# Optimization experiments

Measured on AMD Instinct MI355X. Metric: run time of the kernel, lower is better.

The kernel has to match this reference:

```python
import jax, jax.numpy as jnp
import numpy as np
import math

DIM = 1024
NUM_HEADS = 16
HEAD_DIM = DIM // NUM_HEADS
B, S = 2, 2048

def setup_inputs() -> dict:
    key = jax.random.key(0)
    ks = jax.random.split(key, 9)
    sc = 0.02
    return {
        "x": jax.random.normal(ks[0], (B, S, DIM), jnp.float32),
        "Wq": jax.random.normal(ks[1], (DIM, DIM), jnp.float32) * sc,
        "bq": jax.random.normal(ks[2], (DIM,), jnp.float32) * sc,
        "Wk": jax.random.normal(ks[3], (DIM, DIM), jnp.float32) * sc,
        "bk": jax.random.normal(ks[4], (DIM,), jnp.float32) * sc,
        "Wv": jax.random.normal(ks[5], (DIM, DIM), jnp.float32) * sc,
        "bv": jax.random.normal(ks[6], (DIM,), jnp.float32) * sc,
        "Wo": jax.random.normal(ks[7], (DIM, DIM), jnp.float32) * sc,
        "bo": jax.random.normal(ks[8], (DIM,), jnp.float32) * sc,
    }

def reference(x, Wq, bq, Wk, bk, Wv, bv, Wo, bo):
    b, s, d = x.shape
    h, hd = NUM_HEADS, HEAD_DIM
    # qkv projections: [B,S,D] -> [B,H,S,hd]
    def split_heads(t):
        return t.reshape(b, s, h, hd).transpose(0, 2, 1, 3)
    q = split_heads(x @ Wq + bq)
    k = split_heads(x @ Wk + bk)
    v = split_heads(x @ Wv + bv)
    # scores [B,H,S,S], scale, causal mask via where(-10000), softmax
    scores = jnp.einsum('bhqd,bhkd->bhqk', q, k) / math.sqrt(hd)
    causal = jnp.tril(jnp.ones((s, s), dtype=bool))  # [S,S]
    scores = jnp.where(causal[None, None], scores, jnp.asarray(-10000.0, scores.dtype))
    probs = jax.nn.softmax(scores, axis=-1)
    ctx = jnp.einsum('bhqk,bhkd->bhqd', probs, v)
    ctx = ctx.transpose(0, 2, 1, 3).reshape(b, s, d)
    return ctx @ Wo + bo
```

## Files before the change

kernel.cpp:

```cpp
#include <hip/hip_runtime.h>
#include <hip/hip_bf16.h>

#define DIM 1024
#define NUM_HEADS 16
#define HEAD_DIM 64
#define BATCH 2
#define SEQ 2048
#define M_ROWS (BATCH * SEQ)

typedef short bh8 __attribute__((ext_vector_type(8)));
typedef float f32x4 __attribute__((ext_vector_type(4)));
typedef float f32x16 __attribute__((ext_vector_type(16)));

#define SCALE_Q 0.18033688011116016f

#define MFMA16(a, b, c) __builtin_amdgcn_mfma_f32_16x16x32_bf16(a, b, c, 0, 0, 0)
#define MFMA32(a, b, c) __builtin_amdgcn_mfma_f32_32x32x16_bf16(a, b, c, 0, 0, 0)

#if __has_builtin(__builtin_amdgcn_exp2f)
#define EXP2F(x) __builtin_amdgcn_exp2f(x)
#else
#define EXP2F(x) exp2f(x)
#endif

__device__ __forceinline__ ushort f2bf(float f) {
    union { float f; unsigned u; } v; v.f = f;
    unsigned u = v.u;
    unsigned r = (u + 0x7FFFu + ((u >> 16) & 1u)) >> 16;
    return (ushort)r;
}

__device__ __forceinline__ unsigned cvt_pk_bf16(float lo, float hi) {
    unsigned r;
    asm("v_cvt_pk_bf16_f32 %0, %1, %2" : "=v"(r) : "v"(lo), "v"(hi));
    return r;
}

__device__ __forceinline__ void plane_swap(unsigned a, unsigned b,
                                           unsigned& o0, unsigned& o1, int h) {
#if __has_builtin(__builtin_amdgcn_permlane32_swap)
    (void)h;
    auto pr = __builtin_amdgcn_permlane32_swap(a, b, false, false);
    unsigned o[2]; __builtin_memcpy(o, &pr, 8);
    o0 = o[0]; o1 = o[1];
#else
    unsigned sa = (unsigned)__shfl_xor((int)a, 32);
    unsigned sb = (unsigned)__shfl_xor((int)b, 32);
    o0 = h ? sb : a;
    o1 = h ? b : sa;
#endif
}

__device__ __forceinline__ void async_cp16(const ushort* g, ushort* l) {
    __builtin_amdgcn_global_load_lds(
        (const __attribute__((address_space(1))) void*)(uintptr_t)g,
        (__attribute__((address_space(3))) void*)(uint32_t)(uintptr_t)l,
        16, 0, 0);
}

__global__ __launch_bounds__(256) void prep_inputs(
    const float* __restrict__ W0, const float* __restrict__ W1,
    const float* __restrict__ W2, const float* __restrict__ W3,
    const float* __restrict__ x,
    ushort* __restrict__ T0, ushort* __restrict__ T1,
    ushort* __restrict__ T2, ushort* __restrict__ T3,
    ushort* __restrict__ xb)
{
    const int z = blockIdx.z;
    const int t = threadIdx.x;
    if (z == 4) {
        int base = (blockIdx.y * 32 + blockIdx.x) * 1024 + t;
        const float4* in4 = (const float4*)x;
        ushort4* out4 = (ushort4*)xb;
        #pragma unroll
        for (int i = 0; i < 4; ++i) {
            float4 v = in4[base + i * 256];
            ushort4 o;
            o.x = f2bf(v.x); o.y = f2bf(v.y); o.z = f2bf(v.z); o.w = f2bf(v.w);
            out4[base + i * 256] = o;
        }
        return;
    }
    __shared__ float tile[32][33];
    const float* W = (z == 0) ? W0 : (z == 1) ? W1 : (z == 2) ? W2 : W3;
    ushort* Wt = (z == 0) ? T0 : (z == 1) ? T1 : (z == 2) ? T2 : T3;
    const int tx = t & 31, ty = t >> 5;
    const int k0 = blockIdx.y * 32, n0 = blockIdx.x * 32;
    #pragma unroll
    for (int i = 0; i < 4; ++i)
        tile[ty + 8 * i][tx] = W[(size_t)(k0 + ty + 8 * i) * DIM + n0 + tx];
    __syncthreads();
    #pragma unroll
    for (int i = 0; i < 4; ++i)
        Wt[(size_t)(n0 + ty + 8 * i) * DIM + k0 + tx] = f2bf(tile[tx][ty + 8 * i]);
}

#define GTM 128
#define GTN 64
#define GBK 64

__device__ __forceinline__ void gemm_core(
    const ushort* __restrict__ A, const ushort* __restrict__ Bt,
    ushort* smem, int m0, int n0, int t, f32x4 acc[4][2])
{
    ushort* As = smem;
    ushort* Bs = smem + 8192;
    const int lane = t & 63, wave = t >> 6;
    const int col = lane & 15, quad = lane >> 4;
    const int wm = (wave & 1) * 64, wn = (wave >> 1) * 32;

    for (int k0 = 0; k0 < DIM; k0 += GBK) {
        __syncthreads();
        #pragma unroll
        for (int j = 0; j < 4; ++j) {
            int C = wave * 256 + j * 64 + lane;
            int row = C >> 3;
            int lch = (C & 7) ^ (row & 7);
            async_cp16(&A[(size_t)(m0 + row) * DIM + k0 + lch * 8],
                       &As[(wave * 256 + j * 64) * 8]);
        }
        #pragma unroll
        for (int j = 0; j < 2; ++j) {
            int C = wave * 128 + j * 64 + lane;
            int row = C >> 3;
            int lch = (C & 7) ^ (row & 7);
            async_cp16(&Bt[(size_t)(n0 + row) * DIM + k0 + lch * 8],
                       &Bs[(wave * 128 + j * 64) * 8]);
        }
        __syncthreads();
        #pragma unroll
        for (int kk = 0; kk < 2; ++kk) {
            bh8 af[4], bfr[2];
            #pragma unroll
            for (int mi = 0; mi < 4; ++mi) {
                int row = wm + mi * 16 + col;
                af[mi] = *(const bh8*)&As[row * 64 + (((kk * 4 + quad) ^ (row & 7)) * 8)];
            }
            #pragma unroll
            for (int ni = 0; ni < 2; ++ni) {
                int row = wn + ni * 16 + col;
                bfr[ni] = *(const bh8*)&Bs[row * 64 + (((kk * 4 + quad) ^ (row & 7)) * 8)];
            }
            #pragma unroll
            for (int mi = 0; mi < 4; ++mi)
                #pragma unroll
                for (int ni = 0; ni < 2; ++ni)
                    acc[mi][ni] = MFMA16(af[mi], bfr[ni], acc[mi][ni]);
        }
    }
}

__global__ __launch_bounds__(256) void gemm_qkv(
    const ushort* __restrict__ A,
    const ushort* __restrict__ WqT, const ushort* __restrict__ WkT,
    const ushort* __restrict__ WvT,
    const float* __restrict__ bq, const float* __restrict__ bk,
    const float* __restrict__ bv,
    ushort* __restrict__ qo, ushort* __restrict__ ko_, ushort* __restrict__ vo)
{
    __shared__ ushort smem[12288];
    const int z = blockIdx.z;
    const ushort* Bt = (z == 0) ? WqT : (z == 1) ? WkT : WvT;
    const float* bias = (z == 0) ? bq : (z == 1) ? bk : bv;
    ushort* outp = (z == 0) ? qo : (z == 1) ? ko_ : vo;

    const int t = threadIdx.x;
    const int lane = t & 63, wave = t >> 6;
    const int col = lane & 15, quad = lane >> 4;
    const int m0 = blockIdx.y * GTM, n0 = blockIdx.x * GTN;
    const int wm = (wave & 1) * 64, wn = (wave >> 1) * 32;
    f32x4 acc[4][2] = {};

    gemm_core(A, Bt, smem, m0, n0, t, acc);

    const int b = m0 >> 11, s0 = m0 & (SEQ - 1);
    const int h = n0 >> 6;

    if (z < 2) {
        const float scl = (z == 0) ? SCALE_Q : 1.f;
        __syncthreads();
        ushort* LT = smem;
        #pragma unroll
        for (int mi = 0; mi < 4; ++mi)
            #pragma unroll
            for (int ni = 0; ni < 2; ++ni) {
                int dl = wn + ni * 16 + col;
                float bvv = bias[n0 + dl];
                #pragma unroll
                for (int r = 0; r < 4; ++r) {
                    int ml = wm + mi * 16 + quad * 4 + r;
                    LT[ml * 72 + dl] = f2bf((acc[mi][ni][r] + bvv) * scl);
                }
            }
        __syncthreads();
        ushort* Cp = outp + (((size_t)(b * NUM_HEADS + h) * SEQ + s0) << 6);
        #pragma unroll
        for (int i = 0; i < 4; ++i) {
            int c = i * 256 + t;
            int row = c >> 3, ko = (c & 7) * 8;
            *(uint4*)&Cp[row * 64 + ko] = *(const uint4*)&LT[row * 72 + ko];
        }
    } else {
        __syncthreads();
        ushort* LT = smem;
        #pragma unroll
        for (int mi = 0; mi < 4; ++mi)
            #pragma unroll
            for (int ni = 0; ni < 2; ++ni) {
                int nl = wn + ni * 16 + col;
                float bvv = bias[n0 + nl];
                #pragma unroll
                for (int r = 0; r < 4; ++r) {
                    int ml = wm + mi * 16 + quad * 4 + r;
                    LT[nl * 136 + ml] = f2bf(acc[mi][ni][r] + bvv);
                }
            }
        __syncthreads();
        ushort* Cp = outp + (((size_t)(b * NUM_HEADS + h) * HEAD_DIM) << 11);
        #pragma unroll
        for (int i = 0; i < 4; ++i) {
            int c = i * 256 + t;
            int row = c >> 4, mo = (c & 15) * 8;
            *(uint4*)&Cp[((size_t)row << 11) + s0 + mo] = *(const uint4*)&LT[row * 136 + mo];
        }
    }
}

__global__ __launch_bounds__(256) void gemm_out(
    const ushort* __restrict__ A, const ushort* __restrict__ Bt,
    const float* __restrict__ bias, float* __restrict__ C)
{
    __shared__ ushort smem[12288];
    const int t = threadIdx.x;
    const int lane = t & 63, wave = t >> 6;
    const int col = lane & 15, quad = lane >> 4;
    const int m0 = blockIdx.y * GTM, n0 = blockIdx.x * GTN;
    const int wm = (wave & 1) * 64, wn = (wave >> 1) * 32;
    f32x4 acc[4][2] = {};

    gemm_core(A, Bt, smem, m0, n0, t, acc);

    #pragma unroll
    for (int mi = 0; mi < 4; ++mi)
        #pragma unroll
        for (int ni = 0; ni < 2; ++ni) {
            int n = n0 + wn + ni * 16 + col;
            float bvv = bias[n];
            #pragma unroll
            for (int r = 0; r < 4; ++r) {
                int m = m0 + wm + mi * 16 + quad * 4 + r;
                C[(size_t)m * DIM + n] = acc[mi][ni][r] + bvv;
            }
        }
}

__global__ __launch_bounds__(256, 2) void attn_mfma(
    const ushort* __restrict__ Qg, const ushort* __restrict__ Kg,
    const ushort* __restrict__ Vtg, ushort* __restrict__ ctx)
{
    __shared__ char smem[34304];
    float* OA   = (float*)smem;
    float* OB   = (float*)(smem + 16640);
    float* lbuf = (float*)(smem + 33280);

    const int t = threadIdx.x;
    const int lane = t & 63, wave = t >> 6;
    const int q32 = lane & 31, h = lane >> 5;
    const int bh = blockIdx.x & 31;
    const int pi = blockIdx.x >> 5;
    const int b = bh >> 4, hd = bh & 15;
    const int kw0 = wave * 32;
    const ushort* Kp = Kg + ((size_t)bh << 17);
    const ushort* Vp = Vtg + ((size_t)bh << 17);
    const ushort* Qp0 = Qg + ((size_t)bh << 17);

    #pragma unroll 1
    for (int ph = 0; ph < 2; ++ph) {
        const int qt = ph ? pi : (31 - pi);
        const int q0 = qt << 6;

        bh8 qf[2][4];
        #pragma unroll
        for (int qti = 0; qti < 2; ++qti)
            #pragma unroll
            for (int kc = 0; kc < 4; ++kc)
                qf[qti][kc] = *(const bh8*)&Qp0[((size_t)(q0 + qti * 32 + q32) << 6)
                                                + kc * 16 + h * 8];

        f32x16 O[2][2] = {};
        float l[2] = {0.f, 0.f};
        const int nIter = (q0 + 191) >> 7;

        bh8 kf_n[4], vf_n[2][2];
        #pragma unroll
        for (int kc = 0; kc < 4; ++kc)
            kf_n[kc] = *(const bh8*)&Kp[((size_t)(kw0 + q32) << 6) + kc * 16 + h * 8];
        #pragma unroll
        for (int dti = 0; dti < 2; ++dti)
            #pragma unroll
            for (int kc = 0; kc < 2; ++kc)
                vf_n[dti][kc] = *(const bh8*)&Vp[((size_t)(dti * 32 + q32) << 11)
                                                 + kw0 + kc * 16 + h * 8];

        #pragma unroll 1
        for (int it = 0; it < nIter; ++it) {
            const int kb = it << 7;
            bh8 kf[4], vf[2][2];
            #pragma unroll
            for (int kc = 0; kc < 4; ++kc) kf[kc] = kf_n[kc];
            #pragma unroll
            for (int dti = 0; dti < 2; ++dti) {
                vf[dti][0] = vf_n[dti][0]; vf[dti][1] = vf_n[dti][1];
            }

            if (it + 1 < nIter) {
                const int kb2 = kb + 128;
                #pragma unroll
                for (int kc = 0; kc < 4; ++kc)
                    kf_n[kc] = *(const bh8*)&Kp[((size_t)(kb2 + kw0 + q32) << 6)
                                                + kc * 16 + h * 8];
                #pragma unroll
                for (int dti = 0; dti < 2; ++dti)
                    #pragma unroll
                    for (int kc = 0; kc < 2; ++kc)
                        vf_n[dti][kc] = *(const bh8*)&Vp[((size_t)(dti * 32 + q32) << 11)
                                                         + kb2 + kw0 + kc * 16 + h * 8];
            }

            if (kb + kw0 > q0 + 63) continue;

            f32x16 St[2] = {};
            #pragma unroll
            for (int kc = 0; kc < 4; ++kc) {
                St[0] = MFMA32(kf[kc], qf[0][kc], St[0]);
                St[1] = MFMA32(kf[kc], qf[1][kc], St[1]);
            }

            if (kb + kw0 + 31 > q0) {
                #pragma unroll
                for (int qti = 0; qti < 2; ++qti) {
                    int q_abs = q0 + qti * 32 + q32;
                    #pragma unroll
                    for (int r = 0; r < 16; ++r) {
                        int key_abs = kb + kw0 + (r & 3) + ((r >> 2) << 3) + 4 * h;
                        if (key_abs > q_abs) St[qti][r] = -1e30f;
                    }
                }
            }

            #pragma unroll
            for (int qti = 0; qti < 2; ++qti) {
                float p[16];
                #pragma unroll
                for (int r = 0; r < 16; ++r) p[r] = EXP2F(St[qti][r]);
                float t0 = (p[0] + p[1]) + (p[2] + p[3]);
                float t1 = (p[4] + p[5]) + (p[6] + p[7]);
                float t2 = (p[8] + p[9]) + (p[10] + p[11]);
                float t3 = (p[12] + p[13]) + (p[14] + p[15]);
                l[qti] += (t0 + t1) + (t2 + t3);

                unsigned w[8];
                #pragma unroll
                for (int m = 0; m < 8; ++m) w[m] = cvt_pk_bf16(p[2 * m], p[2 * m + 1]);
                unsigned j0, j1, j2, j3, j4, j5, j6, j7;
                plane_swap(w[0], w[2], j0, j2, h);
                plane_swap(w[1], w[3], j1, j3, h);
                plane_swap(w[4], w[6], j4, j6, h);
                plane_swap(w[5], w[7], j5, j7, h);
                union { unsigned u[4]; bh8 v; } pu0, pu1;
                pu0.u[0] = j0; pu0.u[1] = j1; pu0.u[2] = j2; pu0.u[3] = j3;
                pu1.u[0] = j4; pu1.u[1] = j5; pu1.u[2] = j6; pu1.u[3] = j7;

                O[qti][0] = MFMA32(vf[0][0], pu0.v, O[qti][0]);
                O[qti][1] = MFMA32(vf[1][0], pu0.v, O[qti][1]);
                O[qti][0] = MFMA32(vf[0][1], pu1.v, O[qti][0]);
                O[qti][1] = MFMA32(vf[1][1], pu1.v, O[qti][1]);
            }
        }

        l[0] += __shfl_xor(l[0], 32);
        l[1] += __shfl_xor(l[1], 32);
        if (lane < 32) {
            lbuf[wave * 64 + q32]      = l[0];
            lbuf[wave * 64 + 32 + q32] = l[1];
        }
        __syncthreads();

        if (wave == 1 || wave == 3) {
            float* dst = (wave == 1) ? OA : OB;
            #pragma unroll
            for (int qti = 0; qti < 2; ++qti)
                #pragma unroll
                for (int dti = 0; dti < 2; ++dti)
                    #pragma unroll
                    for (int r = 0; r < 16; ++r) {
                        int d_l = dti * 32 + (r & 3) + ((r >> 2) << 3) + 4 * h;
                        dst[d_l * 65 + qti * 32 + q32] = O[qti][dti][r];
                    }
        }
        __syncthreads();
        if (wave == 0 || wave == 2) {
            float* src = (wave == 0) ? OA : OB;
            #pragma unroll
            for (int qti = 0; qti < 2; ++qti)
                #pragma unroll
                for (int dti = 0; dti < 2; ++dti)
                    #pragma unroll
                    for (int r = 0; r < 16; ++r) {
                        int d_l = dti * 32 + (r & 3) + ((r >> 2) << 3) + 4 * h;
                        O[qti][dti][r] += src[d_l * 65 + qti * 32 + q32];
                    }
        }
        __syncthreads();
        if (wave == 2) {
            #pragma unroll
            for (int qti = 0; qti < 2; ++qti)
                #pragma unroll
                for (int dti = 0; dti < 2; ++dti)
                    #pragma unroll
                    for (int r = 0; r < 16; ++r) {
                        int d_l = dti * 32 + (r & 3) + ((r >> 2) << 3) + 4 * h;
                        OA[d_l * 65 + qti * 32 + q32] = O[qti][dti][r];
                    }
        }
        __syncthreads();
        if (wave == 0) {
            float tot0 = lbuf[q32] + lbuf[64 + q32] + lbuf[128 + q32] + lbuf[192 + q32];
            float tot1 = lbuf[32 + q32] + lbuf[96 + q32] + lbuf[160 + q32] + lbuf[224 + q32];
            float inv0 = 1.f / tot0, inv1 = 1.f / tot1;
            ushort* Oq = (ushort*)(smem + 16640);
            #pragma unroll
            for (int qti = 0; qti < 2; ++qti) {
                float invq = qti ? inv1 : inv0;
                int qrow = qti * 32 + q32;
                #pragma unroll
                for (int dti = 0; dti < 2; ++dti)
                    #pragma unroll
                    for (int rg = 0; rg < 4; ++rg) {
                        int d0 = dti * 32 + rg * 8 + 4 * h;
                        float s0 = (O[qti][dti][rg * 4 + 0] + OA[(d0 + 0) * 65 + qrow]) * invq;
                        float s1 = (O[qti][dti][rg * 4 + 1] + OA[(d0 + 1) * 65 + qrow]) * invq;
                        float s2 = (O[qti][dti][rg * 4 + 2] + OA[(d0 + 2) * 65 + qrow]) * invq;
                        float s3 = (O[qti][dti][rg * 4 + 3] + OA[(d0 + 3) * 65 + qrow]) * invq;
                        uint2 pk; pk.x = cvt_pk_bf16(s0, s1); pk.y = cvt_pk_bf16(s2, s3);
                        *(uint2*)&Oq[qrow * 72 + d0] = pk;
                    }
            }
            #pragma unroll
            for (int i = 0; i < 8; ++i) {
                int c = i * 64 + lane;
                int row = c >> 3, ko = (c & 7) * 8;
                *(uint4*)&ctx[((size_t)(b * SEQ) + q0 + row) * DIM + (hd << 6) + ko] =
                    *(const uint4*)&Oq[row * 72 + ko];
            }
        }
        __syncthreads();
    }
}

extern "C" void kernel_launch(void* const* d_in, const int* in_sizes, int n_in,
                              void* d_out, int out_size, void* d_ws, size_t ws_size,
                              hipStream_t stream) {
    const float* x  = (const float*)d_in[0];
    const float* Wq = (const float*)d_in[1];
    const float* bq = (const float*)d_in[2];
    const float* Wk = (const float*)d_in[3];
    const float* bk = (const float*)d_in[4];
    const float* Wv = (const float*)d_in[5];
    const float* bv = (const float*)d_in[6];
    const float* Wo = (const float*)d_in[7];
    const float* bo = (const float*)d_in[8];
    float* out = (float*)d_out;

    ushort* x_bf   = (ushort*)d_ws;
    ushort* wq_t   = x_bf + 4194304;
    ushort* wk_t   = wq_t + 1048576;
    ushort* wv_t   = wk_t + 1048576;
    ushort* wo_t   = wv_t + 1048576;
    ushort* q_ws   = wo_t + 1048576;
    ushort* k_ws   = q_ws + 4194304;
    ushort* vt_ws  = k_ws + 4194304;
    ushort* ctx_ws = vt_ws + 4194304;

    dim3 pgrid(32, 32, 5);
    prep_inputs<<<pgrid, 256, 0, stream>>>(Wq, Wk, Wv, Wo, x,
                                           wq_t, wk_t, wv_t, wo_t, x_bf);

    dim3 qkv_grid(DIM / GTN, M_ROWS / GTM, 3);
    gemm_qkv<<<qkv_grid, 256, 0, stream>>>(x_bf, wq_t, wk_t, wv_t,
                                           bq, bk, bv, q_ws, k_ws, vt_ws);

    attn_mfma<<<512, 256, 0, stream>>>(q_ws, k_ws, vt_ws, ctx_ws);

    dim3 ogrid(DIM / GTN, M_ROWS / GTM);
    gemm_out<<<ogrid, 256, 0, stream>>>(ctx_ws, wo_t, bo, out);
}
```

Measured before the change: 192.1 us.

## Shrink attention query tile to 32 rows, launch 4x more blocks, drop phase pairing

The attention kernel now gives each block a single 32-row query tile instead of two paired 64-row tiles, and the grid grows from 512 to 2048 blocks. Shared memory is halved and launch bounds raised to 4 blocks per SM to lift occupancy. Heaviest tiles are scheduled first to balance the causal triangle, and the loop now breaks early instead of continuing. K/V are reloaded into the same registers rather than double-buffered, but each block reuses K/V across only half as many queries, so per-row K/V traffic goes up.

```diff
diff --git a/kernel.cpp b/kernel.cpp
--- a/kernel.cpp
+++ b/kernel.cpp
@@ -254,207 +254,169 @@
         }
 }
 
-__global__ __launch_bounds__(256, 2) void attn_mfma(
+__global__ __launch_bounds__(256, 4) void attn_mfma(
     const ushort* __restrict__ Qg, const ushort* __restrict__ Kg,
     const ushort* __restrict__ Vtg, ushort* __restrict__ ctx)
 {
-    __shared__ char smem[34304];
+    __shared__ char smem[17408];
     float* OA   = (float*)smem;
-    float* OB   = (float*)(smem + 16640);
-    float* lbuf = (float*)(smem + 33280);
+    float* OB   = (float*)(smem + 8448);
+    float* lbuf = (float*)(smem + 16896);
 
     const int t = threadIdx.x;
     const int lane = t & 63, wave = t >> 6;
     const int q32 = lane & 31, h = lane >> 5;
     const int bh = blockIdx.x & 31;
-    const int pi = blockIdx.x >> 5;
+    const int qt = 63 - (blockIdx.x >> 5);
     const int b = bh >> 4, hd = bh & 15;
+    const int q0 = qt << 5;
     const int kw0 = wave * 32;
     const ushort* Kp = Kg + ((size_t)bh << 17);
     const ushort* Vp = Vtg + ((size_t)bh << 17);
-    const ushort* Qp0 = Qg + ((size_t)bh << 17);
+    const ushort* Qp = Qg + ((size_t)bh << 17);
+
+    bh8 qf[4];
+    #pragma unroll
+    for (int kc = 0; kc < 4; ++kc)
+        qf[kc] = *(const bh8*)&Qp[((size_t)(q0 + q32) << 6) + kc * 16 + h * 8];
+
+    f32x16 O[2] = {};
+    float l = 0.f;
+    const int nIter = (q0 + 159) >> 7;
+
+    bh8 kf[4], vf[2][2];
+    #pragma unroll
+    for (int kc = 0; kc < 4; ++kc)
+        kf[kc] = *(const bh8*)&Kp[((size_t)(kw0 + q32) << 6) + kc * 16 + h * 8];
+    #pragma unroll
+    for (int dti = 0; dti < 2; ++dti)
+        #pragma unroll
+        for (int kc = 0; kc < 2; ++kc)
+            vf[dti][kc] = *(const bh8*)&Vp[((size_t)(dti * 32 + q32) << 11)
+                                           + kw0 + kc * 16 + h * 8];
 
     #pragma unroll 1
-    for (int ph = 0; ph < 2; ++ph) {
-        const int qt = ph ? pi : (31 - pi);
-        const int q0 = qt << 6;
-
-        bh8 qf[2][4];
-        #pragma unroll
-        for (int qti = 0; qti < 2; ++qti)
+    for (int it = 0; it < nIter; ++it) {
+        const int kb = it << 7;
+        if (kb + kw0 > q0 + 31) break;
+
+        f32x16 St = {};
+        #pragma unroll
+        for (int kc = 0; kc < 4; ++kc)
+            St = MFMA32(kf[kc], qf[kc], St);
+
+        const int kb2 = kb + 128;
+        if (it + 1 < nIter) {
             #pragma unroll
             for (int kc = 0; kc < 4; ++kc)
-                qf[qti][kc] = *(const bh8*)&Qp0[((size_t)(q0 + qti * 32 + q32) << 6)
-                                                + kc * 16 + h * 8];
-
-        f32x16 O[2][2] = {};
-        float l[2] = {0.f, 0.f};
-        const int nIter = (q0 + 191) >> 7;
-
-        bh8 kf_n[4], vf_n[2][2];
-        #pragma unroll
-        for (int kc = 0; kc < 4; ++kc)
-            kf_n[kc] = *(const bh8*)&Kp[((size_t)(kw0 + q32) << 6) + kc * 16 + h * 8];
+                kf[kc] = *(const bh8*)&Kp[((size_t)(kb2 + kw0 + q32) << 6)
+                                          + kc * 16 + h * 8];
+        }
+
+        if (kb + kw0 + 31 > q0) {
+            int q_abs = q0 + q32;
+            #pragma unroll
+            for (int r = 0; r < 16; ++r) {
+                int key_abs = kb + kw0 + (r & 3) + ((r >> 2) << 3) + 4 * h;
+                if (key_abs > q_abs) St[r] = -1e30f;
+            }
+        }
+
+        float p[16];
+        #pragma unroll
+        for (int r = 0; r < 16; ++r) p[r] = EXP2F(St[r]);
+        float t0 = (p[0] + p[1]) + (p[2] + p[3]);
+        float t1 = (p[4] + p[5]) + (p[6] + p[7]);
+        float t2 = (p[8] + p[9]) + (p[10] + p[11]);
+        float t3 = (p[12] + p[13]) + (p[14] + p[15]);
+        l += (t0 + t1) + (t2 + t3);
+
+        unsigned w[8];
+        #pragma unroll
+        for (int m = 0; m < 8; ++m) w[m] = cvt_pk_bf16(p[2 * m], p[2 * m + 1]);
+        unsigned j0, j1, j2, j3, j4, j5, j6, j7;
+        plane_swap(w[0], w[2], j0, j2, h);
+        plane_swap(w[1], w[3], j1, j3, h);
+        plane_swap(w[4], w[6], j4, j6, h);
+        plane_swap(w[5], w[7], j5, j7, h);
+        union { unsigned u[4]; bh8 v; } pu0, pu1;
+        pu0.u[0] = j0; pu0.u[1] = j1; pu0.u[2] = j2; pu0.u[3] = j3;
+        pu1.u[0] = j4; pu1.u[1] = j5; pu1.u[2] = j6; pu1.u[3] = j7;
+
+        O[0] = MFMA32(vf[0][0], pu0.v, O[0]);
+        O[1] = MFMA32(vf[1][0], pu0.v, O[1]);
+        O[0] = MFMA32(vf[0][1], pu1.v, O[0]);
+        O[1] = MFMA32(vf[1][1], pu1.v, O[1]);
+
+        if (it + 1 < nIter) {
+            #pragma unroll
+            for (int dti = 0; dti < 2; ++dti)
+                #pragma unroll
+                for (int kc = 0; kc < 2; ++kc)
+                    vf[dti][kc] = *(const bh8*)&Vp[((size_t)(dti * 32 + q32) << 11)
+                                                   + kb2 + kw0 + kc * 16 + h * 8];
+        }
+    }
+
+    l += __shfl_xor(l, 32);
+    if (h == 0) lbuf[wave * 32 + q32] = l;
+    __syncthreads();
+
+    if (wave == 1 || wave == 3) {
+        float* dst = (wave == 1) ? OA : OB;
         #pragma unroll
         for (int dti = 0; dti < 2; ++dti)
             #pragma unroll
-            for (int kc = 0; kc < 2; ++kc)
-                vf_n[dti][kc] = *(const bh8*)&Vp[((size_t)(dti * 32 + q32) << 11)
-                                                 + kw0 + kc * 16 + h * 8];
-
-        #pragma unroll 1
-        for (int it = 0; it < nIter; ++it) {
-            const int kb = it << 7;
-            bh8 kf[4], vf[2][2];
-            #pragma unroll
-            for (int kc = 0; kc < 4; ++kc) kf[kc] = kf_n[kc];
-            #pragma unroll
-            for (int dti = 0; dti < 2; ++dti) {
-                vf[dti][0] = vf_n[dti][0]; vf[dti][1] = vf_n[dti][1];
-            }
-
-            if (it + 1 < nIter) {
-                const int kb2 = kb + 128;
-                #pragma unroll
-                for (int kc = 0; kc < 4; ++kc)
-                    kf_n[kc] = *(const bh8*)&Kp[((size_t)(kb2 + kw0 + q32) << 6)
-                                                + kc * 16 + h * 8];
-                #pragma unroll
-                for (int dti = 0; dti < 2; ++dti)
-                    #pragma unroll
-                    for (int kc = 0; kc < 2; ++kc)
-                        vf_n[dti][kc] = *(const bh8*)&Vp[((size_t)(dti * 32 + q32) << 11)
-                                                         + kb2 + kw0 + kc * 16 + h * 8];
-            }
-
-            if (kb + kw0 > q0 + 63) continue;
-
-            f32x16 St[2] = {};
-            #pragma unroll
-            for (int kc = 0; kc < 4; ++kc) {
-                St[0] = MFMA32(kf[kc], qf[0][kc], St[0]);
-                St[1] = MFMA32(kf[kc], qf[1][kc], St[1]);
-            }
-
-            if (kb + kw0 + 31 > q0) {
-                #pragma unroll
-                for (int qti = 0; qti < 2; ++qti) {
-                    int q_abs = q0 + qti * 32 + q32;
-                    #pragma unroll
-                    for (int r = 0; r < 16; ++r) {
-                        int key_abs = kb + kw0 + (r & 3) + ((r >> 2) << 3) + 4 * h;
-                        if (key_abs > q_abs) St[qti][r] = -1e30f;
-                    }
-                }
-            }
-
-            #pragma unroll
-            for (int qti = 0; qti < 2; ++qti) {
-                float p[16];
-                #pragma unroll
-                for (int r = 0; r < 16; ++r) p[r] = EXP2F(St[qti][r]);
-                float t0 = (p[0] + p[1]) + (p[2] + p[3]);
-                float t1 = (p[4] + p[5]) + (p[6] + p[7]);
-                float t2 = (p[8] + p[9]) + (p[10] + p[11]);
-                float t3 = (p[12] + p[13]) + (p[14] + p[15]);
-                l[qti] += (t0 + t1) + (t2 + t3);
-
-                unsigned w[8];
-                #pragma unroll
-                for (int m = 0; m < 8; ++m) w[m] = cvt_pk_bf16(p[2 * m], p[2 * m + 1]);
-                unsigned j0, j1, j2, j3, j4, j5, j6, j7;
-                plane_swap(w[0], w[2], j0, j2, h);
-                plane_swap(w[1], w[3], j1, j3, h);
-                plane_swap(w[4], w[6], j4, j6, h);
-                plane_swap(w[5], w[7], j5, j7, h);
-                union { unsigned u[4]; bh8 v; } pu0, pu1;
-                pu0.u[0] = j0; pu0.u[1] = j1; pu0.u[2] = j2; pu0.u[3] = j3;
-                pu1.u[0] = j4; pu1.u[1] = j5; pu1.u[2] = j6; pu1.u[3] = j7;
-
-                O[qti][0] = MFMA32(vf[0][0], pu0.v, O[qti][0]);
-                O[qti][1] = MFMA32(vf[1][0], pu0.v, O[qti][1]);
-                O[qti][0] = MFMA32(vf[0][1], pu1.v, O[qti][0]);
-                O[qti][1] = MFMA32(vf[1][1], pu1.v, O[qti][1]);
-            }
-        }
-
-        l[0] += __shfl_xor(l[0], 32);
-        l[1] += __shfl_xor(l[1], 32);
-        if (lane < 32) {
-            lbuf[wave * 64 + q32]      = l[0];
-            lbuf[wave * 64 + 32 + q32] = l[1];
-        }
-        __syncthreads();
-
-        if (wave == 1 || wave == 3) {
-            float* dst = (wave == 1) ? OA : OB;
-            #pragma unroll
-            for (int qti = 0; qti < 2; ++qti)
-                #pragma unroll
-                for (int dti = 0; dti < 2; ++dti)
-                    #pragma unroll
-                    for (int r = 0; r < 16; ++r) {
-                        int d_l = dti * 32 + (r & 3) + ((r >> 2) << 3) + 4 * h;
-                        dst[d_l * 65 + qti * 32 + q32] = O[qti][dti][r];
-                    }
-        }
-        __syncthreads();
-        if (wave == 0 || wave == 2) {
-            float* src = (wave == 0) ? OA : OB;
-            #pragma unroll
-            for (int qti = 0; qti < 2; ++qti)
-                #pragma unroll
-                for (int dti = 0; dti < 2; ++dti)
-                    #pragma unroll
-                    for (int r = 0; r < 16; ++r) {
-                        int d_l = dti * 32 + (r & 3) + ((r >> 2) << 3) + 4 * h;
-                        O[qti][dti][r] += src[d_l * 65 + qti * 32 + q32];
-                    }
-        }
-        __syncthreads();
-        if (wave == 2) {
-            #pragma unroll
-            for (int qti = 0; qti < 2; ++qti)
-                #pragma unroll
-                for (int dti = 0; dti < 2; ++dti)
-                    #pragma unroll
-                    for (int r = 0; r < 16; ++r) {
-                        int d_l = dti * 32 + (r & 3) + ((r >> 2) << 3) + 4 * h;
-                        OA[d_l * 65 + qti * 32 + q32] = O[qti][dti][r];
-                    }
-        }
-        __syncthreads();
-        if (wave == 0) {
-            float tot0 = lbuf[q32] + lbuf[64 + q32] + lbuf[128 + q32] + lbuf[192 + q32];
-            float tot1 = lbuf[32 + q32] + lbuf[96 + q32] + lbuf[160 + q32] + lbuf[224 + q32];
-            float inv0 = 1.f / tot0, inv1 = 1.f / tot1;
-            ushort* Oq = (ushort*)(smem + 16640);
-            #pragma unroll
-            for (int qti = 0; qti < 2; ++qti) {
-                float invq = qti ? inv1 : inv0;
-                int qrow = qti * 32 + q32;
-                #pragma unroll
-                for (int dti = 0; dti < 2; ++dti)
-                    #pragma unroll
-                    for (int rg = 0; rg < 4; ++rg) {
-                        int d0 = dti * 32 + rg * 8 + 4 * h;
-                        float s0 = (O[qti][dti][rg * 4 + 0] + OA[(d0 + 0) * 65 + qrow]) * invq;
-                        float s1 = (O[qti][dti][rg * 4 + 1] + OA[(d0 + 1) * 65 + qrow]) * invq;
-                        float s2 = (O[qti][dti][rg * 4 + 2] + OA[(d0 + 2) * 65 + qrow]) * invq;
-                        float s3 = (O[qti][dti][rg * 4 + 3] + OA[(d0 + 3) * 65 + qrow]) * invq;
-                        uint2 pk; pk.x = cvt_pk_bf16(s0, s1); pk.y = cvt_pk_bf16(s2, s3);
-                        *(uint2*)&Oq[qrow * 72 + d0] = pk;
-                    }
-            }
-            #pragma unroll
-            for (int i = 0; i < 8; ++i) {
-                int c = i * 64 + lane;
-                int row = c >> 3, ko = (c & 7) * 8;
-                *(uint4*)&ctx[((size_t)(b * SEQ) + q0 + row) * DIM + (hd << 6) + ko] =
-                    *(const uint4*)&Oq[row * 72 + ko];
-            }
-        }
-        __syncthreads();
+            for (int r = 0; r < 16; ++r) {
+                int d_l = dti * 32 + (r & 3) + ((r >> 2) << 3) + 4 * h;
+                dst[d_l * 33 + q32] = O[dti][r];
+            }
+    }
+    __syncthreads();
+    if (wave == 0 || wave == 2) {
+        float* src = (wave == 0) ? OA : OB;
+        #pragma unroll
+        for (int dti = 0; dti < 2; ++dti)
+            #pragma unroll
+            for (int r = 0; r < 16; ++r) {
+                int d_l = dti * 32 + (r & 3) + ((r >> 2) << 3) + 4 * h;
+                O[dti][r] += src[d_l * 33 + q32];
+            }
+    }
+    __syncthreads();
+    if (wave == 2) {
+        #pragma unroll
+        for (int dti = 0; dti < 2; ++dti)
+            #pragma unroll
+            for (int r = 0; r < 16; ++r) {
+                int d_l = dti * 32 + (r & 3) + ((r >> 2) << 3) + 4 * h;
+                OA[d_l * 33 + q32] = O[dti][r];
+            }
+    }
+    __syncthreads();
+    if (wave == 0) {
+        float tot = lbuf[q32] + lbuf[32 + q32] + lbuf[64 + q32] + lbuf[96 + q32];
+        float inv = 1.f / tot;
+        ushort* Oq = (ushort*)(smem + 8448);
+        #pragma unroll
+        for (int dti = 0; dti < 2; ++dti)
+            #pragma unroll
+            for (int rg = 0; rg < 4; ++rg) {
+                int d0 = dti * 32 + rg * 8 + 4 * h;
+                float s0 = (O[dti][rg * 4 + 0] + OA[(d0 + 0) * 33 + q32]) * inv;
+                float s1 = (O[dti][rg * 4 + 1] + OA[(d0 + 1) * 33 + q32]) * inv;
+                float s2 = (O[dti][rg * 4 + 2] + OA[(d0 + 2) * 33 + q32]) * inv;
+                float s3 = (O[dti][rg * 4 + 3] + OA[(d0 + 3) * 33 + q32]) * inv;
+                uint2 pk; pk.x = cvt_pk_bf16(s0, s1); pk.y = cvt_pk_bf16(s2, s3);
+                *(uint2*)&Oq[q32 * 72 + d0] = pk;
+            }
+        #pragma unroll
+        for (int i = 0; i < 4; ++i) {
+            int c = i * 64 + lane;
+            int row = c >> 3, ko = (c & 7) * 8;
+            *(uint4*)&ctx[((size_t)(b * SEQ) + q0 + row) * DIM + (hd << 6) + ko] =
+                *(const uint4*)&Oq[row * 72 + ko];
+        }
     }
 }
 
@@ -490,7 +452,7 @@
     gemm_qkv<<<qkv_grid, 256, 0, stream>>>(x_bf, wq_t, wk_t, wv_t,
                                            bq, bk, bv, q_ws, k_ws, vt_ws);
 
-    attn_mfma<<<512, 256, 0, stream>>>(q_ws, k_ws, vt_ws, ctx_ws);
+    attn_mfma<<<2048, 256, 0, stream>>>(q_ws, k_ws, vt_ws, ctx_ws);
 
     dim3 ogrid(DIM / GTN, M_ROWS / GTM);
     gemm_out<<<ogrid, 256, 0, stream>>>(ctx_ws, wo_t, bo, out);
```

New measurement: 209.2 us. 8.9% more time.

## Split paired attention q-tiles into separate blocks and swizzle GEMM block order

Applied to the files above, without the earlier changes.

The attention kernel previously had each block process two q-tiles (a long and a short one, for causal load balancing). It now launches 1024 blocks that each handle a single q-tile, ordered longest-first, and breaks out of the key loop early instead of continuing. The V prefetch is moved after the PV MFMAs to shorten register live ranges. The QKV and output GEMMs remap block indices with an XCD-style swizzle so that neighbouring tiles land on the same chiplet and share L2. The cost is lost explicit pairing, with load balance left to the hardware scheduler.

```diff
diff --git a/kernel.cpp b/kernel.cpp
--- a/kernel.cpp
+++ b/kernel.cpp
@@ -159,7 +159,10 @@
     ushort* __restrict__ qo, ushort* __restrict__ ko_, ushort* __restrict__ vo)
 {
     __shared__ ushort smem[12288];
-    const int z = blockIdx.z;
+    const int lin = blockIdx.x + 16 * blockIdx.y + 512 * blockIdx.z;
+    const int swz = (lin & 7) * 192 + (lin >> 3);
+    const int bx = swz & 15, by = (swz >> 4) & 31, z = swz >> 9;
+
     const ushort* Bt = (z == 0) ? WqT : (z == 1) ? WkT : WvT;
     const float* bias = (z == 0) ? bq : (z == 1) ? bk : bv;
     ushort* outp = (z == 0) ? qo : (z == 1) ? ko_ : vo;
@@ -167,7 +170,7 @@
     const int t = threadIdx.x;
     const int lane = t & 63, wave = t >> 6;
     const int col = lane & 15, quad = lane >> 4;
-    const int m0 = blockIdx.y * GTM, n0 = blockIdx.x * GTN;
+    const int m0 = by * GTM, n0 = bx * GTN;
     const int wm = (wave & 1) * 64, wn = (wave >> 1) * 32;
     f32x4 acc[4][2] = {};
 
@@ -231,10 +234,14 @@
     const float* __restrict__ bias, float* __restrict__ C)
 {
     __shared__ ushort smem[12288];
+    const int lin = blockIdx.x + 16 * blockIdx.y;
+    const int swz = (lin & 7) * 64 + (lin >> 3);
+    const int bx = swz & 15, by = swz >> 4;
+
     const int t = threadIdx.x;
     const int lane = t & 63, wave = t >> 6;
     const int col = lane & 15, quad = lane >> 4;
-    const int m0 = blockIdx.y * GTM, n0 = blockIdx.x * GTN;
+    const int m0 = by * GTM, n0 = bx * GTN;
     const int wm = (wave & 1) * 64, wn = (wave >> 1) * 32;
     f32x4 acc[4][2] = {};
 
@@ -267,194 +274,187 @@
     const int lane = t & 63, wave = t >> 6;
     const int q32 = lane & 31, h = lane >> 5;
     const int bh = blockIdx.x & 31;
-    const int pi = blockIdx.x >> 5;
+    const int qt = 31 - (blockIdx.x >> 5);
     const int b = bh >> 4, hd = bh & 15;
+    const int q0 = qt << 6;
     const int kw0 = wave * 32;
     const ushort* Kp = Kg + ((size_t)bh << 17);
     const ushort* Vp = Vtg + ((size_t)bh << 17);
-    const ushort* Qp0 = Qg + ((size_t)bh << 17);
+    const ushort* Qp = Qg + ((size_t)bh << 17);
+
+    bh8 qf[2][4];
+    #pragma unroll
+    for (int qti = 0; qti < 2; ++qti)
+        #pragma unroll
+        for (int kc = 0; kc < 4; ++kc)
+            qf[qti][kc] = *(const bh8*)&Qp[((size_t)(q0 + qti * 32 + q32) << 6)
+                                           + kc * 16 + h * 8];
+
+    f32x16 O[2][2] = {};
+    float l[2] = {0.f, 0.f};
+    const int nIter = (q0 + 191) >> 7;
+
+    bh8 kf_n[4], vf[2][2];
+    #pragma unroll
+    for (int kc = 0; kc < 4; ++kc)
+        kf_n[kc] = *(const bh8*)&Kp[((size_t)(kw0 + q32) << 6) + kc * 16 + h * 8];
+    #pragma unroll
+    for (int dti = 0; dti < 2; ++dti)
+        #pragma unroll
+        for (int kc = 0; kc < 2; ++kc)
+            vf[dti][kc] = *(const bh8*)&Vp[((size_t)(dti * 32 + q32) << 11)
+                                           + kw0 + kc * 16 + h * 8];
 
     #pragma unroll 1
-    for (int ph = 0; ph < 2; ++ph) {
-        const int qt = ph ? pi : (31 - pi);
-        const int q0 = qt << 6;
-
-        bh8 qf[2][4];
+    for (int it = 0; it < nIter; ++it) {
+        const int kb = it << 7;
+        if (kb + kw0 > q0 + 63) break;
+
+        bh8 kf[4];
+        #pragma unroll
+        for (int kc = 0; kc < 4; ++kc) kf[kc] = kf_n[kc];
+
+        const int kb2 = kb + 128;
+        if (it + 1 < nIter) {
+            #pragma unroll
+            for (int kc = 0; kc < 4; ++kc)
+                kf_n[kc] = *(const bh8*)&Kp[((size_t)(kb2 + kw0 + q32) << 6)
+                                            + kc * 16 + h * 8];
+        }
+
+        f32x16 St[2] = {};
+        #pragma unroll
+        for (int kc = 0; kc < 4; ++kc) {
+            St[0] = MFMA32(kf[kc], qf[0][kc], St[0]);
+            St[1] = MFMA32(kf[kc], qf[1][kc], St[1]);
+        }
+
+        if (kb + kw0 + 31 > q0) {
+            #pragma unroll
+            for (int qti = 0; qti < 2; ++qti) {
+                int q_abs = q0 + qti * 32 + q32;
+                #pragma unroll
+                for (int r = 0; r < 16; ++r) {
+                    int key_abs = kb + kw0 + (r & 3) + ((r >> 2) << 3) + 4 * h;
+                    if (key_abs > q_abs) St[qti][r] = -1e30f;
+                }
+            }
+        }
+
+        #pragma unroll
+        for (int qti = 0; qti < 2; ++qti) {
+            float p[16];
+            #pragma unroll
+            for (int r = 0; r < 16; ++r) p[r] = EXP2F(St[qti][r]);
+            float t0 = (p[0] + p[1]) + (p[2] + p[3]);
+            float t1 = (p[4] + p[5]) + (p[6] + p[7]);
+            float t2 = (p[8] + p[9]) + (p[10] + p[11]);
+            float t3 = (p[12] + p[13]) + (p[14] + p[15]);
+            l[qti] += (t0 + t1) + (t2 + t3);
+
+            unsigned w[8];
+            #pragma unroll
+            for (int m = 0; m < 8; ++m) w[m] = cvt_pk_bf16(p[2 * m], p[2 * m + 1]);
+            unsigned j0, j1, j2, j3, j4, j5, j6, j7;
+            plane_swap(w[0], w[2], j0, j2, h);
+            plane_swap(w[1], w[3], j1, j3, h);
+            plane_swap(w[4], w[6], j4, j6, h);
+            plane_swap(w[5], w[7], j5, j7, h);
+            union { unsigned u[4]; bh8 v; } pu0, pu1;
+            pu0.u[0] = j0; pu0.u[1] = j1; pu0.u[2] = j2; pu0.u[3] = j3;
+            pu1.u[0] = j4; pu1.u[1] = j5; pu1.u[2] = j6; pu1.u[3] = j7;
+
+            O[qti][0] = MFMA32(vf[0][0], pu0.v, O[qti][0]);
+            O[qti][1] = MFMA32(vf[1][0], pu0.v, O[qti][1]);
+            O[qti][0] = MFMA32(vf[0][1], pu1.v, O[qti][0]);
+            O[qti][1] = MFMA32(vf[1][1], pu1.v, O[qti][1]);
+        }
+
+        if (it + 1 < nIter) {
+            #pragma unroll
+            for (int dti = 0; dti < 2; ++dti)
+                #pragma unroll
+                for (int kc = 0; kc < 2; ++kc)
+                    vf[dti][kc] = *(const bh8*)&Vp[((size_t)(dti * 32 + q32) << 11)
+                                                   + kb2 + kw0 + kc * 16 + h * 8];
+        }
+    }
+
+    l[0] += __shfl_xor(l[0], 32);
+    l[1] += __shfl_xor(l[1], 32);
+    if (lane < 32) {
+        lbuf[wave * 64 + q32]      = l[0];
+        lbuf[wave * 64 + 32 + q32] = l[1];
+    }
+    __syncthreads();
+
+    if (wave == 1 || wave == 3) {
+        float* dst = (wave == 1) ? OA : OB;
         #pragma unroll
         for (int qti = 0; qti < 2; ++qti)
             #pragma unroll
-            for (int kc = 0; kc < 4; ++kc)
-                qf[qti][kc] = *(const bh8*)&Qp0[((size_t)(q0 + qti * 32 + q32) << 6)
-                                                + kc * 16 + h * 8];
-
-        f32x16 O[2][2] = {};
-        float l[2] = {0.f, 0.f};
-        const int nIter = (q0 + 191) >> 7;
-
-        bh8 kf_n[4], vf_n[2][2];
-        #pragma unroll
-        for (int kc = 0; kc < 4; ++kc)
-            kf_n[kc] = *(const bh8*)&Kp[((size_t)(kw0 + q32) << 6) + kc * 16 + h * 8];
-        #pragma unroll
-        for (int dti = 0; dti < 2; ++dti)
-            #pragma unroll
-            for (int kc = 0; kc < 2; ++kc)
-                vf_n[dti][kc] = *(const bh8*)&Vp[((size_t)(dti * 32 + q32) << 11)
-                                                 + kw0 + kc * 16 + h * 8];
-
-        #pragma unroll 1
-        for (int it = 0; it < nIter; ++it) {
-            const int kb = it << 7;
-            bh8 kf[4], vf[2][2];
-            #pragma unroll
-            for (int kc = 0; kc < 4; ++kc) kf[kc] = kf_n[kc];
-            #pragma unroll
-            for (int dti = 0; dti < 2; ++dti) {
-                vf[dti][0] = vf_n[dti][0]; vf[dti][1] = vf_n[dti][1];
-            }
-
-            if (it + 1 < nIter) {
-                const int kb2 = kb + 128;
-                #pragma unroll
-                for (int kc = 0; kc < 4; ++kc)
-                    kf_n[kc] = *(const bh8*)&Kp[((size_t)(kb2 + kw0 + q32) << 6)
-                                                + kc * 16 + h * 8];
-                #pragma unroll
-                for (int dti = 0; dti < 2; ++dti)
-                    #pragma unroll
-                    for (int kc = 0; kc < 2; ++kc)
-                        vf_n[dti][kc] = *(const bh8*)&Vp[((size_t)(dti * 32 + q32) << 11)
-                                                         + kb2 + kw0 + kc * 16 + h * 8];
-            }
-
-            if (kb + kw0 > q0 + 63) continue;
-
-            f32x16 St[2] = {};
-            #pragma unroll
-            for (int kc = 0; kc < 4; ++kc) {
-                St[0] = MFMA32(kf[kc], qf[0][kc], St[0]);
-                St[1] = MFMA32(kf[kc], qf[1][kc], St[1]);
-            }
-
-            if (kb + kw0 + 31 > q0) {
-                #pragma unroll
-                for (int qti = 0; qti < 2; ++qti) {
-                    int q_abs = q0 + qti * 32 + q32;
-                    #pragma unroll
-                    for (int r = 0; r < 16; ++r) {
-                        int key_abs = kb + kw0 + (r & 3) + ((r >> 2) << 3) + 4 * h;
-                        if (key_abs > q_abs) St[qti][r] = -1e30f;
-                    }
-                }
-            }
-
-            #pragma unroll
-            for (int qti = 0; qti < 2; ++qti) {
-                float p[16];
-                #pragma unroll
-                for (int r = 0; r < 16; ++r) p[r] = EXP2F(St[qti][r]);
-                float t0 = (p[0] + p[1]) + (p[2] + p[3]);
-                float t1 = (p[4] + p[5]) + (p[6] + p[7]);
-                float t2 = (p[8] + p[9]) + (p[10] + p[11]);
-                float t3 = (p[12] + p[13]) + (p[14] + p[15]);
-                l[qti] += (t0 + t1) + (t2 + t3);
-
-                unsigned w[8];
-                #pragma unroll
-                for (int m = 0; m < 8; ++m) w[m] = cvt_pk_bf16(p[2 * m], p[2 * m + 1]);
-                unsigned j0, j1, j2, j3, j4, j5, j6, j7;
-                plane_swap(w[0], w[2], j0, j2, h);
-                plane_swap(w[1], w[3], j1, j3, h);
-                plane_swap(w[4], w[6], j4, j6, h);
-                plane_swap(w[5], w[7], j5, j7, h);
-                union { unsigned u[4]; bh8 v; } pu0, pu1;
-                pu0.u[0] = j0; pu0.u[1] = j1; pu0.u[2] = j2; pu0.u[3] = j3;
-                pu1.u[0] = j4; pu1.u[1] = j5; pu1.u[2] = j6; pu1.u[3] = j7;
-
-                O[qti][0] = MFMA32(vf[0][0], pu0.v, O[qti][0]);
-                O[qti][1] = MFMA32(vf[1][0], pu0.v, O[qti][1]);
-                O[qti][0] = MFMA32(vf[0][1], pu1.v, O[qti][0]);
-                O[qti][1] = MFMA32(vf[1][1], pu1.v, O[qti][1]);
-            }
-        }
-
-        l[0] += __shfl_xor(l[0], 32);
-        l[1] += __shfl_xor(l[1], 32);
-        if (lane < 32) {
-            lbuf[wave * 64 + q32]      = l[0];
-            lbuf[wave * 64 + 32 + q32] = l[1];
-        }
-        __syncthreads();
-
-        if (wave == 1 || wave == 3) {
-            float* dst = (wave == 1) ? OA : OB;
-            #pragma unroll
-            for (int qti = 0; qti < 2; ++qti)
-                #pragma unroll
-                for (int dti = 0; dti < 2; ++dti)
-                    #pragma unroll
-                    for (int r = 0; r < 16; ++r) {
-                        int d_l = dti * 32 + (r & 3) + ((r >> 2) << 3) + 4 * h;
-                        dst[d_l * 65 + qti * 32 + q32] = O[qti][dti][r];
-                    }
-        }
-        __syncthreads();
-        if (wave == 0 || wave == 2) {
-            float* src = (wave == 0) ? OA : OB;
-            #pragma unroll
-            for (int qti = 0; qti < 2; ++qti)
-                #pragma unroll
-                for (int dti = 0; dti < 2; ++dti)
-                    #pragma unroll
-                    for (int r = 0; r < 16; ++r) {
-                        int d_l = dti * 32 + (r & 3) + ((r >> 2) << 3) + 4 * h;
-                        O[qti][dti][r] += src[d_l * 65 + qti * 32 + q32];
-                    }
-        }
-        __syncthreads();
-        if (wave == 2) {
-            #pragma unroll
-            for (int qti = 0; qti < 2; ++qti)
-                #pragma unroll
-                for (int dti = 0; dti < 2; ++dti)
-                    #pragma unroll
-                    for (int r = 0; r < 16; ++r) {
-                        int d_l = dti * 32 + (r & 3) + ((r >> 2) << 3) + 4 * h;
-                        OA[d_l * 65 + qti * 32 + q32] = O[qti][dti][r];
-                    }
-        }
-        __syncthreads();
-        if (wave == 0) {
-            float tot0 = lbuf[q32] + lbuf[64 + q32] + lbuf[128 + q32] + lbuf[192 + q32];
-            float tot1 = lbuf[32 + q32] + lbuf[96 + q32] + lbuf[160 + q32] + lbuf[224 + q32];
-            float inv0 = 1.f / tot0, inv1 = 1.f / tot1;
-            ushort* Oq = (ushort*)(smem + 16640);
-            #pragma unroll
-            for (int qti = 0; qti < 2; ++qti) {
-                float invq = qti ? inv1 : inv0;
-                int qrow = qti * 32 + q32;
-                #pragma unroll
-                for (int dti = 0; dti < 2; ++dti)
-                    #pragma unroll
-                    for (int rg = 0; rg < 4; ++rg) {
-                        int d0 = dti * 32 + rg * 8 + 4 * h;
-                        float s0 = (O[qti][dti][rg * 4 + 0] + OA[(d0 + 0) * 65 + qrow]) * invq;
-                        float s1 = (O[qti][dti][rg * 4 + 1] + OA[(d0 + 1) * 65 + qrow]) * invq;
-                        float s2 = (O[qti][dti][rg * 4 + 2] + OA[(d0 + 2) * 65 + qrow]) * invq;
-                        float s3 = (O[qti][dti][rg * 4 + 3] + OA[(d0 + 3) * 65 + qrow]) * invq;
-                        uint2 pk; pk.x = cvt_pk_bf16(s0, s1); pk.y = cvt_pk_bf16(s2, s3);
-                        *(uint2*)&Oq[qrow * 72 + d0] = pk;
-                    }
-            }
-            #pragma unroll
-            for (int i = 0; i < 8; ++i) {
-                int c = i * 64 + lane;
-                int row = c >> 3, ko = (c & 7) * 8;
-                *(uint4*)&ctx[((size_t)(b * SEQ) + q0 + row) * DIM + (hd << 6) + ko] =
-                    *(const uint4*)&Oq[row * 72 + ko];
-            }
-        }
-        __syncthreads();
+            for (int dti = 0; dti < 2; ++dti)
+                #pragma unroll
+                for (int r = 0; r < 16; ++r) {
+                    int d_l = dti * 32 + (r & 3) + ((r >> 2) << 3) + 4 * h;
+                    dst[d_l * 65 + qti * 32 + q32] = O[qti][dti][r];
+                }
+    }
+    __syncthreads();
+    if (wave == 0 || wave == 2) {
+        float* src = (wave == 0) ? OA : OB;
+        #pragma unroll
+        for (int qti = 0; qti < 2; ++qti)
+            #pragma unroll
+            for (int dti = 0; dti < 2; ++dti)
+                #pragma unroll
+                for (int r = 0; r < 16; ++r) {
+                    int d_l = dti * 32 + (r & 3) + ((r >> 2) << 3) + 4 * h;
+                    O[qti][dti][r] += src[d_l * 65 + qti * 32 + q32];
+                }
+    }
+    __syncthreads();
+    if (wave == 2) {
+        #pragma unroll
+        for (int qti = 0; qti < 2; ++qti)
+            #pragma unroll
+            for (int dti = 0; dti < 2; ++dti)
+                #pragma unroll
+                for (int r = 0; r < 16; ++r) {
+                    int d_l = dti * 32 + (r & 3) + ((r >> 2) << 3) + 4 * h;
+                    OA[d_l * 65 + qti * 32 + q32] = O[qti][dti][r];
+                }
+    }
+    __syncthreads();
+    if (wave == 0) {
+        float tot0 = lbuf[q32] + lbuf[64 + q32] + lbuf[128 + q32] + lbuf[192 + q32];
+        float tot1 = lbuf[32 + q32] + lbuf[96 + q32] + lbuf[160 + q32] + lbuf[224 + q32];
+        float inv0 = 1.f / tot0, inv1 = 1.f / tot1;
+        ushort* Oq = (ushort*)(smem + 16640);
+        #pragma unroll
+        for (int qti = 0; qti < 2; ++qti) {
+            float invq = qti ? inv1 : inv0;
+            int qrow = qti * 32 + q32;
+            #pragma unroll
+            for (int dti = 0; dti < 2; ++dti)
+                #pragma unroll
+                for (int rg = 0; rg < 4; ++rg) {
+                    int d0 = dti * 32 + rg * 8 + 4 * h;
+                    float s0 = (O[qti][dti][rg * 4 + 0] + OA[(d0 + 0) * 65 + qrow]) * invq;
+                    float s1 = (O[qti][dti][rg * 4 + 1] + OA[(d0 + 1) * 65 + qrow]) * invq;
+                    float s2 = (O[qti][dti][rg * 4 + 2] + OA[(d0 + 2) * 65 + qrow]) * invq;
+                    float s3 = (O[qti][dti][rg * 4 + 3] + OA[(d0 + 3) * 65 + qrow]) * invq;
+                    uint2 pk; pk.x = cvt_pk_bf16(s0, s1); pk.y = cvt_pk_bf16(s2, s3);
+                    *(uint2*)&Oq[qrow * 72 + d0] = pk;
+                }
+        }
+        #pragma unroll
+        for (int i = 0; i < 8; ++i) {
+            int c = i * 64 + lane;
+            int row = c >> 3, ko = (c & 7) * 8;
+            *(uint4*)&ctx[((size_t)(b * SEQ) + q0 + row) * DIM + (hd << 6) + ko] =
+                *(const uint4*)&Oq[row * 72 + ko];
+        }
     }
 }
 
@@ -490,7 +490,7 @@
     gemm_qkv<<<qkv_grid, 256, 0, stream>>>(x_bf, wq_t, wk_t, wv_t,
                                            bq, bk, bv, q_ws, k_ws, vt_ws);
 
-    attn_mfma<<<512, 256, 0, stream>>>(q_ws, k_ws, vt_ws, ctx_ws);
+    attn_mfma<<<1024, 256, 0, stream>>>(q_ws, k_ws, vt_ws, ctx_ws);
 
     dim3 ogrid(DIM / GTN, M_ROWS / GTM);
     gemm_out<<<ogrid, 256, 0, stream>>>(ctx_ws, wo_t, bo, out);
```

Result: faster. 184.9 us (-3.8%).
